# Kernel optimization log

Measured on AMD Instinct MI355X. Metric: run time of the kernel, lower is better.

The kernel has to match this reference:

```python
import jax, jax.numpy as jnp
import numpy as np

# Dimensions
F = 512      # features = len(in_degrees)
D = 64
S, B, N = 1, 64, 256   # outer sample dim, hyper-batch, points per batch element
C = 128      # conditioner (phi) feature dim
P = F * F + F  # flat params per batch element: weight + bias


def _mask():
    # hidden-layer MADE degrees: arange(F) % max(1, D-1) + min(1, D-1)
    d = jnp.arange(F) % (D - 1) + 1
    # MaskedLinear hidden mask: out_degrees[:, None] >= in_degrees[None, :]
    # (the torch code reshapes the square [F,F] mask, which is an identity
    #  memory reshape, so element (i, j) = (d[i] >= d[j]))
    return (d[:, None] >= d[None, :]).astype(jnp.float32)


def setup_inputs() -> dict:
    key = jax.random.key(0)
    k1, k2, k3, k4 = jax.random.split(key, 4)
    return {
        "inputs": jax.random.normal(k1, (S, B, N, F), jnp.float32),
        "phi": jax.random.normal(k2, (S, B, C), jnp.float32),
        "Wc": jax.random.normal(k3, (P, C), jnp.float32) * 0.02,
        "bc": jax.random.normal(k4, (P,), jnp.float32) * 0.02,
    }


def reference(inputs, phi, Wc, bc):
    # Conditioner net: linear hypernetwork phi -> flat per-batch params.
    params = jnp.einsum('sbc,pc->sbp', phi, Wc) + bc          # [S,B,P]
    w = params[..., : F * F].reshape(S, B, F, F)               # [S,B,F_in,F_out]
    b = params[..., F * F : F * F + F]                         # [S,B,F]
    mw = w * _mask()                                           # masked per-batch weights

    # Residual block (no batch norm, dropout p=0): act -> masked linear (x2) -> residual
    t = jax.nn.relu(inputs)
    t = jnp.einsum('sbni,sbik->sbnk', t, mw) + b[:, :, None, :]
    t = jax.nn.relu(t)
    # Both MaskedLinear layers split the SAME conditioner output, so they share
    # (w, b); only the masks could differ, and with these degrees they coincide.
    t = jnp.einsum('sbni,sbik->sbnk', t, mw) + b[:, :, None, :]
    return inputs + t
```

## Files before the change

### kernel.cpp

```cpp
#include <hip/hip_runtime.h>
#include <hip/hip_bf16.h>

#define F_   512
#define FF_  (512 * 512)
#define C_   128

typedef __attribute__((ext_vector_type(4))) float f32x4;
typedef __attribute__((ext_vector_type(8))) short s16x8;
typedef __attribute__((ext_vector_type(4))) unsigned short u16x4;

__device__ __forceinline__ unsigned short f2bf(float f) {
    union { __hip_bfloat16 h; unsigned short u; } c;
    c.h = __float2bfloat16(f);
    return c.u;
}

__device__ __forceinline__ s16x8 pack8(f32x4 lo, f32x4 hi) {
    s16x8 r;
    r[0] = (short)f2bf(lo[0]); r[1] = (short)f2bf(lo[1]);
    r[2] = (short)f2bf(lo[2]); r[3] = (short)f2bf(lo[3]);
    r[4] = (short)f2bf(hi[0]); r[5] = (short)f2bf(hi[1]);
    r[6] = (short)f2bf(hi[2]); r[7] = (short)f2bf(hi[3]);
    return r;
}

#define GLDS16(gp, lp)                                                         \
    __builtin_amdgcn_global_load_lds(                                          \
        (const __attribute__((address_space(1))) void*)(gp),                   \
        (__attribute__((address_space(3))) void*)(lp), 16, 0, 0)

__global__ __launch_bounds__(256) void k0_prepack(
    const float* __restrict__ phi, unsigned short* __restrict__ phiP)
{
    const int t = threadIdx.x;
#pragma unroll
    for (int j = 0; j < 4; ++j) {
        int e = (j << 8) + t;
        int lane = e & 63, mk = e >> 6;
        int m = mk >> 2, kk = mk & 3;
        int brow = lane & 15, quad = lane >> 4;
        const float* p = phi + ((m << 4) + brow) * C_ + kk * 32 + (quad << 3);
        s16x8 v = pack8(*(const f32x4*)p, *(const f32x4*)(p + 4));
        *(s16x8*)&phiP[e << 3] = v;
    }
}

__global__ __launch_bounds__(256, 2) void k1_params(
    const unsigned short* __restrict__ phiP, const float* __restrict__ Wc,
    const float* __restrict__ bc, unsigned short* __restrict__ wT,
    float* __restrict__ biasWS, const float* __restrict__ phi)
{
    const int blk = blockIdx.x;
    const int tid = threadIdx.x;

    if (blk >= 512) {
        int g = ((blk - 512) << 8) + tid;
        int k = g >> 6, b = g & 63;
        const f32x4* w4 = (const f32x4*)(Wc + (size_t)(FF_ + k) * C_);
        const f32x4* p4 = (const f32x4*)(phi + b * C_);
        float acc = bc[FF_ + k];
#pragma unroll
        for (int c = 0; c < 32; ++c) {
            f32x4 a = w4[c], q = p4[c];
            acc += a[0]*q[0] + a[1]*q[1] + a[2]*q[2] + a[3]*q[3];
        }
        biasWS[(b << 9) + k] = acc;
        return;
    }

    __shared__ __align__(16) char stg[4][2][8192];
    __shared__ __align__(16) unsigned short trans[4][64 * 24];

    const int lane = tid & 63, wave = tid >> 6, quad = lane >> 4;
    const int kgrp = blk & 63, igrp = blk >> 6;
    const int k0 = kgrp << 3;
    const int kw = k0 + (wave << 1);
    const int ibase = igrp << 6;

    s16x8 afr[4][4];
#pragma unroll
    for (int mk = 0; mk < 16; ++mk)
        afr[mk >> 2][mk & 3] = *(const s16x8*)&phiP[((mk << 6) + lane) << 3];

    const int c = lane & 15, il = c & 7, kl = c >> 3;
    const int kcell = kw + kl;
    const int dkc = kcell % 63;
    const int dk0 = kw % 63, dk1 = (kw + 1) % 63;
    const int dmin = dk0 < dk1 ? dk0 : dk1;

    float bcv[8];
    unsigned keepm = 0;
#pragma unroll
    for (int t = 0; t < 8; ++t) {
        int icell = ibase + (t << 3) + il;
        bcv[t] = bc[icell * F_ + kcell];
        if ((icell % 63) >= dkc) keepm |= 1u << t;
    }

    const int rsel  = lane >> 5;
    const int sslot = (lane & 31) << 4;

    auto STAGE = [&](int t, int buf) {
        const int i0 = ibase + (t << 3);
#pragma unroll
        for (int g = 0; g < 8; ++g) {
            int r = i0 + g;
            int srow = ((r % 63) >= dmin) ? r : i0;
            const char* src =
                (const char*)(Wc + ((size_t)srow * F_ + kw + rsel) * C_)
                + (sslot ^ (g << 4));
            GLDS16(src, &stg[wave][buf][g << 10]);
        }
    };

    STAGE(0, 0);

#pragma unroll
    for (int t = 0; t < 8; ++t) {
        if (t < 7) STAGE(t + 1, (t + 1) & 1);
        if (t < 7) asm volatile("s_waitcnt vmcnt(8)" ::: "memory");
        else       asm volatile("s_waitcnt vmcnt(0)" ::: "memory");

        f32x4 acc[4];
#pragma unroll
        for (int m = 0; m < 4; ++m) acc[m] = (f32x4){0.f, 0.f, 0.f, 0.f};

        const char* rowp = &stg[wave][t & 1][(il << 10) + (kl << 9)];
#pragma unroll
        for (int kk = 0; kk < 4; ++kk) {
            int y0 = (kk << 7) + (((quad << 5) | 0)  ^ (il << 4));
            int y1 = (kk << 7) + (((quad << 5) | 16) ^ (il << 4));
            s16x8 bfr = pack8(*(const f32x4*)(rowp + y0),
                              *(const f32x4*)(rowp + y1));
#pragma unroll
            for (int m = 0; m < 4; ++m)
                acc[m] = __builtin_amdgcn_mfma_f32_16x16x32_bf16(
                    afr[m][kk], bfr, acc[m], 0, 0, 0);
        }

        const bool keep = (keepm >> t) & 1;
        const float bv = bcv[t];
#pragma unroll
        for (int m = 0; m < 4; ++m)
#pragma unroll
            for (int r = 0; r < 4; ++r) {
                int b = (m << 4) + (quad << 2) + r;
                trans[wave][b * 24 + (kl << 3) + il] =
                    keep ? f2bf(acc[m][r] + bv) : (unsigned short)0;
            }

        {
            const int i0 = ibase + (t << 3);
            s16x8 c0 = *(const s16x8*)&trans[wave][lane * 24];
            s16x8 c1 = *(const s16x8*)&trans[wave][lane * 24 + 8];
            *(s16x8*)&wT[(((size_t)((lane << 9) + kw))     << 9) + i0] = c0;
            *(s16x8*)&wT[(((size_t)((lane << 9) + kw + 1)) << 9) + i0] = c1;
        }
    }
}

#define SMEM_BOFF 66560
#define CHUNK_B   32768
#define SMEM_TOT  (66560 + 2 * 32768)

__global__ __launch_bounds__(512) void k2_apply(
    const float* __restrict__ X, const unsigned short* __restrict__ wT,
    const float* __restrict__ biasWS, float* __restrict__ out)
{
    extern __shared__ char smem[];
    unsigned short* A_lds = (unsigned short*)smem;

    const int blk = blockIdx.x;
    const int sw  = ((blk & 7) << 5) + (blk >> 3);
    const int b   = sw >> 2;
    const int n0  = (sw & 3) << 6;

    const int tid = threadIdx.x, lane = tid & 63, wave = tid >> 6;
    const int wn = wave >> 2, wk = wave & 3;

    const float* Xb = X + (((size_t)(b * 256 + n0)) << 9);
    float*       Ob = out + (((size_t)(b * 256 + n0)) << 9);
    const unsigned short* wTb = wT + ((size_t)b << 18);

    float biasr[8];
#pragma unroll
    for (int nt = 0; nt < 8; ++nt)
        biasr[nt] = biasWS[(b << 9) + (wk << 7) + (nt << 4) + (lane & 15)];

    {
        const f32x4* X4 = (const f32x4*)Xb;
#pragma unroll
        for (int j = 0; j < 16; ++j) {
            int f = (j << 9) + tid;
            int row = f >> 7, c4 = f & 127;
            f32x4 v = X4[f];
            u16x4 h;
#pragma unroll
            for (int e = 0; e < 4; ++e) h[e] = f2bf(fmaxf(v[e], 0.f));
            *(u16x4*)&A_lds[row * 520 + (c4 << 2)] = h;
        }
    }

    const int srcslot = ((lane & 3) ^ ((lane >> 3) & 3)) << 3;

    f32x4 acc[2][8];

    for (int phase = 0; phase < 2; ++phase) {
#pragma unroll
        for (int mt = 0; mt < 2; ++mt)
#pragma unroll
            for (int nt = 0; nt < 8; ++nt) acc[mt][nt] = (f32x4){0.f, 0.f, 0.f, 0.f};

#pragma unroll
        for (int g = 0; g < 4; ++g) {
            int krow = (wave << 6) + (g << 4) + (lane >> 2);
            const unsigned short* src = wTb + ((size_t)krow << 9) + srcslot;
            char* lp = smem + SMEM_BOFF + (((wave << 6) + (g << 4)) << 6);
            GLDS16(src, lp);
        }
        asm volatile("s_waitcnt vmcnt(0)" ::: "memory");
        __syncthreads();

        for (int c = 0; c < 16; ++c) {
            const int cur = c & 1;
            if (c < 15) {
                const int i0n = (c + 1) << 5;
#pragma unroll
                for (int g = 0; g < 4; ++g) {
                    int krow = (wave << 6) + (g << 4) + (lane >> 2);
                    const unsigned short* src = wTb + ((size_t)krow << 9) + i0n + srcslot;
                    char* lp = smem + SMEM_BOFF + (cur ^ 1) * CHUNK_B
                             + (((wave << 6) + (g << 4)) << 6);
                    GLDS16(src, lp);
                }
            }
            const int i0c = c << 5;
            s16x8 afr[2];
#pragma unroll
            for (int mt = 0; mt < 2; ++mt) {
                int n = (wn << 5) + (mt << 4) + (lane & 15);
                afr[mt] = *(const s16x8*)&A_lds[n * 520 + i0c + ((lane >> 4) << 3)];
            }
            const unsigned short* Bb =
                (const unsigned short*)(smem + SMEM_BOFF + cur * CHUNK_B);
#pragma unroll
            for (int nt = 0; nt < 8; ++nt) {
                int k = (wk << 7) + (nt << 4) + (lane & 15);
                int slot = (((lane >> 4) ^ ((k >> 1) & 3)) << 3);
                s16x8 bfr = *(const s16x8*)&Bb[(k << 5) + slot];
#pragma unroll
                for (int mt = 0; mt < 2; ++mt)
                    acc[mt][nt] = __builtin_amdgcn_mfma_f32_16x16x32_bf16(
                        afr[mt], bfr, acc[mt][nt], 0, 0, 0);
            }
            asm volatile("s_waitcnt vmcnt(0)" ::: "memory");
            __syncthreads();
        }

        if (phase == 0) {
#pragma unroll
            for (int mt = 0; mt < 2; ++mt)
#pragma unroll
                for (int nt = 0; nt < 8; ++nt) {
                    int k = (wk << 7) + (nt << 4) + (lane & 15);
#pragma unroll
                    for (int r = 0; r < 4; ++r) {
                        int n = (wn << 5) + (mt << 4) + ((lane >> 4) << 2) + r;
                        A_lds[n * 520 + k] =
                            f2bf(fmaxf(acc[mt][nt][r] + biasr[nt], 0.f));
                    }
                }
            __syncthreads();
        }
    }

#pragma unroll
    for (int mt = 0; mt < 2; ++mt)
#pragma unroll
        for (int nt = 0; nt < 8; ++nt) {
            int k = (wk << 7) + (nt << 4) + (lane & 15);
#pragma unroll
            for (int r = 0; r < 4; ++r) {
                int n = (wn << 5) + (mt << 4) + ((lane >> 4) << 2) + r;
                size_t off = ((size_t)n << 9) + k;
                Ob[off] = Xb[off] + acc[mt][nt][r] + biasr[nt];
            }
        }
}

extern "C" void kernel_launch(void* const* d_in, const int* in_sizes, int n_in,
                              void* d_out, int out_size, void* d_ws, size_t ws_size,
                              hipStream_t stream) {
    const float* inputs = (const float*)d_in[0];
    const float* phi    = (const float*)d_in[1];
    const float* Wc     = (const float*)d_in[2];
    const float* bc     = (const float*)d_in[3];
    float* out = (float*)d_out;

    unsigned short* wT = (unsigned short*)d_ws;
    float* biasWS = (float*)((char*)d_ws + (size_t)64 * 512 * 512 * 2);
    unsigned short* phiP =
        (unsigned short*)((char*)d_ws + (size_t)64 * 512 * 512 * 2 + 64 * 512 * 4);

    hipLaunchKernelGGL(k0_prepack, dim3(1), dim3(256), 0, stream, phi, phiP);

    hipLaunchKernelGGL(k1_params, dim3(640), dim3(256), 0, stream,
                       phiP, Wc, bc, wT, biasWS, phi);

    hipFuncSetAttribute((const void*)k2_apply,
                        hipFuncAttributeMaxDynamicSharedMemorySize, SMEM_TOT);
    hipLaunchKernelGGL(k2_apply, dim3(256), dim3(512), SMEM_TOT, stream,
                       inputs, wT, biasWS, out);
}
```

Baseline: 86.47 us.

## Retile hypernetwork weight kernel to emit transposed bf16 directly and skip masked tiles

```diff
diff --git a/kernel.cpp b/kernel.cpp
--- a/kernel.cpp
+++ b/kernel.cpp
@@ -69,92 +69,122 @@
     }
 
     __shared__ __align__(16) char stg[4][2][8192];
-    __shared__ __align__(16) unsigned short trans[4][64 * 24];
 
     const int lane = tid & 63, wave = tid >> 6, quad = lane >> 4;
-    const int kgrp = blk & 63, igrp = blk >> 6;
-    const int k0 = kgrp << 3;
-    const int kw = k0 + (wave << 1);
-    const int ibase = igrp << 6;
-
-    s16x8 afr[4][4];
+    const int w  = (blk << 2) + wave;
+    const int i0 = (w & 31) << 4;
+    const int k0 = (w >> 5) << 3;
+
+    s16x8 bfrP[4][4];
 #pragma unroll
     for (int mk = 0; mk < 16; ++mk)
-        afr[mk >> 2][mk & 3] = *(const s16x8*)&phiP[((mk << 6) + lane) << 3];
-
-    const int c = lane & 15, il = c & 7, kl = c >> 3;
-    const int kcell = kw + kl;
-    const int dkc = kcell % 63;
-    const int dk0 = kw % 63, dk1 = (kw + 1) % 63;
-    const int dmin = dk0 < dk1 ? dk0 : dk1;
-
-    float bcv[8];
+        bfrP[mk >> 2][mk & 3] = *(const s16x8*)&phiP[((mk << 6) + lane) << 3];
+
+    f32x4 biasv[4][2];
+#pragma unroll
+    for (int rr = 0; rr < 4; ++rr) {
+        const float* p = bc + (i0 + (quad << 2) + rr) * F_ + k0;
+        biasv[rr][0] = *(const f32x4*)p;
+        biasv[rr][1] = *(const f32x4*)(p + 4);
+    }
+
     unsigned keepm = 0;
-#pragma unroll
-    for (int t = 0; t < 8; ++t) {
-        int icell = ibase + (t << 3) + il;
-        bcv[t] = bc[icell * F_ + kcell];
-        if ((icell % 63) >= dkc) keepm |= 1u << t;
-    }
-
-    const int rsel  = lane >> 5;
-    const int sslot = (lane & 31) << 4;
-
-    auto STAGE = [&](int t, int buf) {
-        const int i0 = ibase + (t << 3);
-#pragma unroll
-        for (int g = 0; g < 8; ++g) {
-            int r = i0 + g;
-            int srow = ((r % 63) >= dmin) ? r : i0;
-            const char* src =
-                (const char*)(Wc + ((size_t)srow * F_ + kw + rsel) * C_)
-                + (sslot ^ (g << 4));
-            GLDS16(src, &stg[wave][buf][g << 10]);
+    {
+#pragma unroll
+        for (int ct = 0; ct < 8; ++ct) {
+            int dk = (k0 + ct) % 63;
+#pragma unroll
+            for (int rr = 0; rr < 4; ++rr) {
+                int di = (i0 + (quad << 2) + rr) % 63;
+                if (di >= dk) keepm |= 1u << ((ct << 2) + rr);
+            }
+        }
+    }
+    int maxd = i0 % 63 + 15; maxd = maxd > 62 ? 62 : maxd;
+    unsigned skipm = 0;
+#pragma unroll
+    for (int ct = 0; ct < 8; ++ct)
+        if (((k0 + ct) % 63) > maxd) skipm |= 1u << ct;
+
+    const int r2 = lane >> 5, s = lane & 31;
+    char* const stw0 = stg[wave][0];
+    char* const stw1 = stg[wave][1];
+
+    auto STAGE = [&](int ct, char* dst) {
+        const bool sk = (skipm >> ct) & 1;
+        const int  k  = k0 + ct;
+#pragma unroll
+        for (int j = 0; j < 8; ++j) {
+            int row = (j << 1) + r2;
+            int isrc = sk ? i0 : (i0 + row);
+            const char* src = (const char*)(Wc + ((size_t)(isrc * F_ + k)) * C_)
+                            + ((s << 4) ^ ((row & 7) << 6));
+            GLDS16(src, dst + (row << 9) + ((s << 4) ^ ((row & 7) << 6)));
         }
     };
 
-    STAGE(0, 0);
-
-#pragma unroll
-    for (int t = 0; t < 8; ++t) {
-        if (t < 7) STAGE(t + 1, (t + 1) & 1);
-        if (t < 7) asm volatile("s_waitcnt vmcnt(8)" ::: "memory");
-        else       asm volatile("s_waitcnt vmcnt(0)" ::: "memory");
+    asm volatile("s_waitcnt vmcnt(0)" ::: "memory");
+
+    auto STAGE2 = [&](int ct, char* dst) {
+        const bool sk = (skipm >> ct) & 1;
+        const int  k  = k0 + ct;
+#pragma unroll
+        for (int j = 0; j < 8; ++j) {
+            int row = (j << 1) + r2;
+            int isrc = sk ? i0 : (i0 + row);
+            const char* src = (const char*)(Wc + ((size_t)(isrc * F_ + k)) * C_)
+                            + ((s << 4) ^ ((row & 7) << 6));
+            GLDS16(src, dst + (j << 10));
+        }
+    };
+    (void)STAGE;
+
+    STAGE2(0, stw0);
+
+#pragma unroll
+    for (int ct = 0; ct < 8; ++ct) {
+        char* bufc = (ct & 1) ? stw1 : stw0;
+        if (ct < 7) STAGE2(ct + 1, (ct & 1) ? stw0 : stw1);
+
+        if (ct == 0)      asm volatile("s_waitcnt vmcnt(8)"  ::: "memory");
+        else if (ct < 7)  asm volatile("s_waitcnt vmcnt(12)" ::: "memory");
+        else              asm volatile("s_waitcnt vmcnt(4)"  ::: "memory");
+        __builtin_amdgcn_sched_barrier(0);
 
         f32x4 acc[4];
 #pragma unroll
-        for (int m = 0; m < 4; ++m) acc[m] = (f32x4){0.f, 0.f, 0.f, 0.f};
-
-        const char* rowp = &stg[wave][t & 1][(il << 10) + (kl << 9)];
-#pragma unroll
-        for (int kk = 0; kk < 4; ++kk) {
-            int y0 = (kk << 7) + (((quad << 5) | 0)  ^ (il << 4));
-            int y1 = (kk << 7) + (((quad << 5) | 16) ^ (il << 4));
-            s16x8 bfr = pack8(*(const f32x4*)(rowp + y0),
-                              *(const f32x4*)(rowp + y1));
-#pragma unroll
-            for (int m = 0; m < 4; ++m)
-                acc[m] = __builtin_amdgcn_mfma_f32_16x16x32_bf16(
-                    afr[m][kk], bfr, acc[m], 0, 0, 0);
-        }
-
-        const bool keep = (keepm >> t) & 1;
-        const float bv = bcv[t];
-#pragma unroll
-        for (int m = 0; m < 4; ++m)
-#pragma unroll
-            for (int r = 0; r < 4; ++r) {
-                int b = (m << 4) + (quad << 2) + r;
-                trans[wave][b * 24 + (kl << 3) + il] =
-                    keep ? f2bf(acc[m][r] + bv) : (unsigned short)0;
-            }
-
-        {
-            const int i0 = ibase + (t << 3);
-            s16x8 c0 = *(const s16x8*)&trans[wave][lane * 24];
-            s16x8 c1 = *(const s16x8*)&trans[wave][lane * 24 + 8];
-            *(s16x8*)&wT[(((size_t)((lane << 9) + kw))     << 9) + i0] = c0;
-            *(s16x8*)&wT[(((size_t)((lane << 9) + kw + 1)) << 9) + i0] = c1;
+        for (int bt = 0; bt < 4; ++bt) acc[bt] = (f32x4){0.f, 0.f, 0.f, 0.f};
+
+        const bool sk = (skipm >> ct) & 1;
+        if (!sk) {
+            const int rowB = (lane & 15) << 9;
+            const int swz  = (lane & 7) << 6;
+#pragma unroll
+            for (int kk = 0; kk < 4; ++kk) {
+                int x0 = ((kk << 7) + (quad << 5)) ^ swz;
+                int x1 = ((kk << 7) + (quad << 5) + 16) ^ swz;
+                f32x4 lo = *(const f32x4*)(bufc + rowB + x0);
+                f32x4 hi = *(const f32x4*)(bufc + rowB + x1);
+                s16x8 aW = pack8(lo, hi);
+#pragma unroll
+                for (int bt = 0; bt < 4; ++bt)
+                    acc[bt] = __builtin_amdgcn_mfma_f32_16x16x32_bf16(
+                        aW, bfrP[bt][kk], acc[bt], 0, 0, 0);
+            }
+        }
+
+        const int k = k0 + ct;
+#pragma unroll
+        for (int bt = 0; bt < 4; ++bt) {
+            u16x4 v;
+#pragma unroll
+            for (int rr = 0; rr < 4; ++rr) {
+                bool kp = (!sk) && ((keepm >> ((ct << 2) + rr)) & 1);
+                float bv = (ct < 4) ? biasv[rr][0][ct] : biasv[rr][1][ct - 4];
+                v[rr] = kp ? f2bf(acc[bt][rr] + bv) : (unsigned short)0;
+            }
+            int b = (bt << 4) + (lane & 15);
+            *(u16x4*)&wT[(((size_t)((b << 9) + k)) << 9) + i0 + (quad << 2)] = v;
         }
     }
 }
```

After: 71.81 us (median of 2 runs). -16.9%, faster.

## Restructure weight-generation kernel to share staged Wc tiles across waves

Applied to the files above, without the earlier changes.

```diff
diff --git a/kernel.cpp b/kernel.cpp
--- a/kernel.cpp
+++ b/kernel.cpp
@@ -68,93 +68,115 @@
         return;
     }
 
-    __shared__ __align__(16) char stg[4][2][8192];
-    __shared__ __align__(16) unsigned short trans[4][64 * 24];
+    __shared__ __align__(16) char stg[2][32768];
+    __shared__ __align__(16) unsigned short trans[4][1280];
+    __shared__ float bcs[64 * 9];
 
     const int lane = tid & 63, wave = tid >> 6, quad = lane >> 4;
-    const int kgrp = blk & 63, igrp = blk >> 6;
-    const int k0 = kgrp << 3;
-    const int kw = k0 + (wave << 1);
-    const int ibase = igrp << 6;
-
-    s16x8 afr[4][4];
-#pragma unroll
-    for (int mk = 0; mk < 16; ++mk)
-        afr[mk >> 2][mk & 3] = *(const s16x8*)&phiP[((mk << 6) + lane) << 3];
-
-    const int c = lane & 15, il = c & 7, kl = c >> 3;
-    const int kcell = kw + kl;
-    const int dkc = kcell % 63;
-    const int dk0 = kw % 63, dk1 = (kw + 1) % 63;
-    const int dmin = dk0 < dk1 ? dk0 : dk1;
-
-    float bcv[8];
-    unsigned keepm = 0;
-#pragma unroll
-    for (int t = 0; t < 8; ++t) {
-        int icell = ibase + (t << 3) + il;
-        bcv[t] = bc[icell * F_ + kcell];
-        if ((icell % 63) >= dkc) keepm |= 1u << t;
-    }
-
-    const int rsel  = lane >> 5;
-    const int sslot = (lane & 31) << 4;
+    const int i0 = (blk >> 6) << 6;
+    const int k0 = (blk & 63) << 3;
+
+    {
+        int il = tid >> 2, kp = (tid & 3) << 1;
+        const float* s = bc + (size_t)(i0 + il) * F_ + k0 + kp;
+        bcs[il * 9 + kp]     = s[0];
+        bcs[il * 9 + kp + 1] = s[1];
+    }
+
+    s16x8 bfr[4];
+#pragma unroll
+    for (int kk = 0; kk < 4; ++kk)
+        bfr[kk] = *(const s16x8*)&phiP[((((wave << 2) + kk) << 6) | lane) << 3];
+
+    int dcell[4][4];
+#pragma unroll
+    for (int mt = 0; mt < 4; ++mt)
+#pragma unroll
+        for (int rr = 0; rr < 4; ++rr)
+            dcell[mt][rr] = (i0 + mt * 16 + (quad << 2) + rr) % 63;
+    int dmax[4];
+#pragma unroll
+    for (int mt = 0; mt < 4; ++mt) {
+        int a = (i0 + mt * 16) % 63;
+        dmax[mt] = (a + 15 >= 63) ? 62 : a + 15;
+    }
+
+    int irow[8], drow[8], swj[8];
+#pragma unroll
+    for (int j = 0; j < 8; ++j) {
+        int rl = (wave << 4) + (j << 1) + (lane >> 5);
+        irow[j] = i0 + rl;
+        drow[j] = (i0 + rl) % 63;
+        swj[j]  = ((lane & 31) << 4) ^ ((rl & 7) << 4);
+    }
+    const int idup = i0 + ((62 - (i0 % 63)) + 63) % 63;
 
     auto STAGE = [&](int t, int buf) {
-        const int i0 = ibase + (t << 3);
-#pragma unroll
-        for (int g = 0; g < 8; ++g) {
-            int r = i0 + g;
-            int srow = ((r % 63) >= dmin) ? r : i0;
-            const char* src =
-                (const char*)(Wc + ((size_t)srow * F_ + kw + rsel) * C_)
-                + (sslot ^ (g << 4));
-            GLDS16(src, &stg[wave][buf][g << 10]);
+        const int k = k0 + t, dk = (k0 + t) % 63;
+#pragma unroll
+        for (int j = 0; j < 8; ++j) {
+            int isel = (drow[j] >= dk) ? irow[j] : idup;
+            const char* src = (const char*)Wc
+                            + ((size_t)(isel * F_ + k) << 9) + swj[j];
+            GLDS16(src, stg[buf] + (((wave << 4) + (j << 1)) << 9));
         }
     };
 
     STAGE(0, 0);
+    __syncthreads();
+
+    const int swz = (lane & 7) << 4;
 
 #pragma unroll
     for (int t = 0; t < 8; ++t) {
         if (t < 7) STAGE(t + 1, (t + 1) & 1);
-        if (t < 7) asm volatile("s_waitcnt vmcnt(8)" ::: "memory");
-        else       asm volatile("s_waitcnt vmcnt(0)" ::: "memory");
-
-        f32x4 acc[4];
-#pragma unroll
-        for (int m = 0; m < 4; ++m) acc[m] = (f32x4){0.f, 0.f, 0.f, 0.f};
-
-        const char* rowp = &stg[wave][t & 1][(il << 10) + (kl << 9)];
-#pragma unroll
-        for (int kk = 0; kk < 4; ++kk) {
-            int y0 = (kk << 7) + (((quad << 5) | 0)  ^ (il << 4));
-            int y1 = (kk << 7) + (((quad << 5) | 16) ^ (il << 4));
-            s16x8 bfr = pack8(*(const f32x4*)(rowp + y0),
-                              *(const f32x4*)(rowp + y1));
-#pragma unroll
-            for (int m = 0; m < 4; ++m)
-                acc[m] = __builtin_amdgcn_mfma_f32_16x16x32_bf16(
-                    afr[m][kk], bfr, acc[m], 0, 0, 0);
-        }
-
-        const bool keep = (keepm >> t) & 1;
-        const float bv = bcv[t];
-#pragma unroll
-        for (int m = 0; m < 4; ++m)
-#pragma unroll
-            for (int r = 0; r < 4; ++r) {
-                int b = (m << 4) + (quad << 2) + r;
-                trans[wave][b * 24 + (kl << 3) + il] =
-                    keep ? f2bf(acc[m][r] + bv) : (unsigned short)0;
-            }
-
-        {
-            const int i0 = ibase + (t << 3);
-            s16x8 c0 = *(const s16x8*)&trans[wave][lane * 24];
-            s16x8 c1 = *(const s16x8*)&trans[wave][lane * 24 + 8];
-            *(s16x8*)&wT[(((size_t)((lane << 9) + kw))     << 9) + i0] = c0;
-            *(s16x8*)&wT[(((size_t)((lane << 9) + kw + 1)) << 9) + i0] = c1;
+
+        const int dk = (k0 + t) % 63;
+        const char* sb = stg[t & 1];
+        unsigned short* trw = trans[wave];
+
+#pragma unroll
+        for (int mt = 0; mt < 4; ++mt) {
+            const int tpos = ((lane & 15) * 160
+                           + ((mt * 32 + (quad << 3)) ^ swz)) >> 1;
+            if (dmax[mt] >= dk) {
+                f32x4 acc = (f32x4){0.f, 0.f, 0.f, 0.f};
+                const char* rowb = sb + ((mt * 16 + (lane & 15)) << 9);
+#pragma unroll
+                for (int kk = 0; kk < 4; ++kk) {
+                    int x = ((kk << 7) + (quad << 5)) ^ swz;
+                    f32x4 lo = *(const f32x4*)(rowb + x);
+                    f32x4 hi = *(const f32x4*)(rowb + (x ^ 16));
+                    acc = __builtin_amdgcn_mfma_f32_16x16x32_bf16(
+                        pack8(lo, hi), bfr[kk], acc, 0, 0, 0);
+                }
+                u16x4 v;
+#pragma unroll
+                for (int rr = 0; rr < 4; ++rr) {
+                    float bv = bcs[(mt * 16 + (quad << 2) + rr) * 9 + t];
+                    v[rr] = (dcell[mt][rr] >= dk)
+                          ? f2bf(acc[rr] + bv) : (unsigned short)0;
+                }
+                *(u16x4*)&trw[tpos] = v;
+            } else {
+                *(u16x4*)&trw[tpos] = (u16x4){0, 0, 0, 0};
+            }
+        }
+
+#pragma unroll
+        for (int h = 0; h < 2; ++h) {
+            int bl = (h << 3) + (lane >> 3), r = lane & 7;
+            int rr2 = r ^ (bl & 7);
+            s16x8 v = *(const s16x8*)&trw[bl * 80 + (rr2 << 3)];
+            unsigned short* dst = wT
+                + (((size_t)(((wave << 4) + bl) << 9) + k0 + t) << 9)
+                + i0 + (r << 3);
+            *(s16x8*)dst = v;
+        }
+
+        if (t < 7) {
+            asm volatile("s_waitcnt vmcnt(2)" ::: "memory");
+            __builtin_amdgcn_s_barrier();
         }
     }
 }
```

Result: faster. 75.06 us (-13.2%).
